# Performance work log

Hardware: AMD Instinct MI355X
Metric: run time of the kernel (lower is better)

The kernel has to match this reference:

```python
import jax, jax.numpy as jnp
import numpy as np

N = 40000      # nodes
E = 640000     # edges
G = 2048       # graphs
D = 128        # emb_dim
T = 10         # num_tasks
L = 5          # layers
ATOM_VOCAB = 64
BOND_VOCAB = 8
BN_EPS = 1e-5


def _bn(x, g, b, m, v):
    # inference-mode BatchNorm1d with running stats
    return (x - m) * jax.lax.rsqrt(v + BN_EPS) * g + b


def setup_inputs() -> dict:
    key = jax.random.key(0)
    ks = jax.random.split(key, 24)
    inp = {
        "x_atom": jax.random.randint(ks[0], (N, 9), 0, ATOM_VOCAB),
        "edge_index": jax.random.randint(ks[1], (2, E), 0, N),
        "edge_attr": jax.random.randint(ks[2], (E, 3), 0, BOND_VOCAB),
        "batch": jnp.sort(jax.random.randint(ks[3], (N,), 0, G)),
        # embedding tables
        "atom_emb": jax.random.normal(ks[4], (9, ATOM_VOCAB, D)) * 0.1,
        "bond_emb": jax.random.normal(ks[5], (L, 3, BOND_VOCAB, D)) * 0.1,
        # per-layer GIN params (stacked over L)
        "eps": jnp.zeros((L,)),
        "W1": jax.random.normal(ks[6], (L, D, 2 * D)) * 0.05,
        "b1": jnp.zeros((L, 2 * D)),
        "g1": jnp.ones((L, 2 * D)),
        "bt1": jnp.zeros((L, 2 * D)),
        "m1": jax.random.normal(ks[7], (L, 2 * D)) * 0.1,
        "v1": jax.random.uniform(ks[8], (L, 2 * D), minval=0.5, maxval=1.5),
        "W2": jax.random.normal(ks[9], (L, 2 * D, D)) * 0.05,
        "b2": jnp.zeros((L, D)),
        # outer BatchNorm per layer
        "gO": jnp.ones((L, D)),
        "btO": jnp.zeros((L, D)),
        "mO": jax.random.normal(ks[10], (L, D)) * 0.1,
        "vO": jax.random.uniform(ks[11], (L, D), minval=0.5, maxval=1.5),
        # prediction head
        "Wp": jax.random.normal(ks[12], (D, T)) * 0.05,
        "bp": jnp.zeros((T,)),
    }
    return inp


def reference(x_atom, edge_index, edge_attr, batch, atom_emb, bond_emb, eps,
              W1, b1, g1, bt1, m1, v1, W2, b2, gO, btO, mO, vO, Wp, bp):
    src, dst = edge_index[0], edge_index[1]
    # AtomEncoder: sum of per-feature embeddings -> [N, D]
    x = atom_emb[jnp.arange(9)[None, :], x_atom].sum(axis=1)
    feat3 = jnp.arange(3)[None, :]
    for i in range(L):
        # BondEncoder for this layer -> [E, D]
        e = bond_emb[i][feat3, edge_attr].sum(axis=1)
        # message: relu(x_j + edge_emb); aggregate: scatter-add at dst
        msg = jax.nn.relu(x[src] + e)
        agg = jax.ops.segment_sum(msg, dst, num_segments=N)
        h = (1.0 + eps[i]) * x + agg
        # MLP: Linear -> BN -> ReLU -> Linear
        h = jax.nn.relu(_bn(h @ W1[i] + b1[i], g1[i], bt1[i], m1[i], v1[i]))
        h = h @ W2[i] + b2[i]
        # outer BN; ReLU after all but last layer (dropout = identity in eval)
        x = _bn(h, gO[i], btO[i], mO[i], vO[i])
        if i < L - 1:
            x = jax.nn.relu(x)
    # global mean pool over graphs
    sums = jax.ops.segment_sum(x, batch, num_segments=G)
    cnt = jax.ops.segment_sum(jnp.ones((N,), x.dtype), batch, num_segments=G)
    pooled = sums / jnp.maximum(cnt, 1.0)[:, None]
    return pooled @ Wp + bp
```

## Files before the change

kernel.cpp:

```cpp
#include <hip/hip_runtime.h>
#include <hip/hip_bf16.h>

#define NN 40000
#define NE 640000
#define NG 2048
#define DD 128
#define NT 10
#define NL 5
#define NB 80

typedef __attribute__((ext_vector_type(8))) short short8;
typedef __attribute__((ext_vector_type(8))) float f32x8;
typedef __attribute__((ext_vector_type(4))) float f32x4;
typedef unsigned short ushort_t;
typedef unsigned char uchar_t;

static __device__ __forceinline__ ushort_t f2b(float f) {
    return __bfloat16_as_ushort(__float2bfloat16(f));
}
static __device__ __forceinline__ float b2f(ushort_t u) {
    return __bfloat162float(__ushort_as_bfloat16(u));
}
static __device__ __forceinline__ uchar_t f2p8(float f) {
    return (uchar_t)(__builtin_amdgcn_cvt_pk_fp8_f32(f, 0.f, 0, false) & 0xFF);
}

__global__ void __launch_bounds__(256)
k_setup(const float* __restrict__ W1, const float* __restrict__ W2,
        const float* __restrict__ bemb, const int* __restrict__ xa,
        const float* __restrict__ aemb, const int* __restrict__ ei,
        ushort_t* __restrict__ W1P, ushort_t* __restrict__ W2P,
        ushort_t* __restrict__ ebsum16, ushort_t* __restrict__ x16,
        uchar_t* __restrict__ x8, int* __restrict__ gcnt) {
    int b = blockIdx.x, t = threadIdx.x;
    if (b < 1280) {
        int tid = b * 256 + t;
        int layer = tid >> 16;
        int r = tid & 65535;
        int half = r >> 15;
        int q = r & 32767;
        int j = q & 7;
        int lane = (q >> 3) & 63;
        if (half == 0) {
            int kk = (q >> 9) & 3;
            int nt = q >> 11;
            int n = nt * 16 + (lane & 15);
            int k = kk * 32 + (lane >> 4) * 8 + j;
            W1P[layer * 32768 + q] = f2b(W1[(layer * DD + k) * 256 + n]);
        } else {
            int kk = (q >> 9) & 7;
            int nt = q >> 12;
            int n = nt * 16 + (lane & 15);
            int k = kk * 32 + (lane >> 4) * 8 + j;
            W2P[layer * 32768 + q] = f2b(W2[(layer * 256 + k) * DD + n]);
        }
        int d = tid & 127;
        int c = (tid >> 7) & 511;
        const float* bl = bemb + (size_t)layer * 3 * 8 * DD;
        ebsum16[tid] = f2b(bl[(c & 7) * DD + d] + bl[(8 + ((c >> 3) & 7)) * DD + d] +
                           bl[(16 + (c >> 6)) * DD + d]);
    } else if (b < 3780) {
        int bb = b - 1280;
        __shared__ int idxS[144];
        if (t < 144) idxS[t] = xa[bb * 144 + t];
        __syncthreads();
        int nl = t >> 4, dcol = t & 15;
        int n = bb * 16 + nl;
        float acc[8];
#pragma unroll
        for (int k = 0; k < 8; ++k) acc[k] = 0.f;
#pragma unroll
        for (int f = 0; f < 9; ++f) {
            const f32x8 v = *(const f32x8*)&aemb[(f * 64 + idxS[nl * 9 + f]) * DD + dcol * 8];
#pragma unroll
            for (int k = 0; k < 8; ++k) acc[k] += v[k];
        }
        short8 o16;
#pragma unroll
        for (int k = 0; k < 8; ++k) o16[k] = (short)f2b(acc[k]);
        *(short8*)&x16[(size_t)n * DD + dcol * 8] = o16;
        unsigned int lo = 0, hi = 0;
        lo = __builtin_amdgcn_cvt_pk_fp8_f32(acc[0], acc[1], lo, false);
        lo = __builtin_amdgcn_cvt_pk_fp8_f32(acc[2], acc[3], lo, true);
        hi = __builtin_amdgcn_cvt_pk_fp8_f32(acc[4], acc[5], hi, false);
        hi = __builtin_amdgcn_cvt_pk_fp8_f32(acc[6], acc[7], hi, true);
        *(uint2*)&x8[(size_t)n * DD + dcol * 8] = make_uint2(lo, hi);
    } else {
        __shared__ int hist[NB];
        int e0 = (b - 3780) * 1024;
        if (t < NB) hist[t] = 0;
        __syncthreads();
#pragma unroll
        for (int k = 0; k < 4; ++k) {
            int e = e0 + k * 256 + t;
            atomicAdd(&hist[ei[NE + e] >> 9], 1);
        }
        __syncthreads();
        if (t < NB) atomicAdd(&gcnt[t], hist[t]);
    }
}

__global__ void __launch_bounds__(256)
k_bucket(const int* __restrict__ ei, const int* __restrict__ ea,
         const int* __restrict__ gcnt, int* __restrict__ gbk,
         int2* __restrict__ ebuf) {
    __shared__ int hist[NB];
    __shared__ int sbase[NB];
    __shared__ int sB[128];
    __shared__ int exS[NB];
    int t = threadIdx.x;
    if (t < NB) hist[t] = 0;
    int v0 = 0;
    if (t < 128) { v0 = (t < NB) ? gcnt[t] : 0; sB[t] = v0; }
    __syncthreads();
    for (int d = 1; d < 128; d <<= 1) {
        int add = (t < 128 && t >= d) ? sB[t - d] : 0;
        __syncthreads();
        if (t < 128) sB[t] += add;
        __syncthreads();
    }
    if (t < NB) exS[t] = sB[t] - v0;
    __syncthreads();
    int e0 = blockIdx.x * 1024;
    int rank[4], buck[4], rec[4], dstv[4];
#pragma unroll
    for (int k = 0; k < 4; ++k) {
        int e = e0 + k * 256 + t;
        int src = ei[e];
        int dst = ei[NE + e];
        int a0 = ea[e * 3 + 0], a1 = ea[e * 3 + 1], a2 = ea[e * 3 + 2];
        rec[k] = src | ((a0 | (a1 << 3) | (a2 << 6)) << 16);
        dstv[k] = dst;
        int b = dst >> 9;
        buck[k] = b;
        rank[k] = atomicAdd(&hist[b], 1);
    }
    __syncthreads();
    if (t < NB) sbase[t] = atomicAdd(&gbk[t], hist[t]);
    __syncthreads();
#pragma unroll
    for (int k = 0; k < 4; ++k) {
        int b = buck[k];
        int slot = exS[b] + sbase[b] + rank[k];
        ebuf[slot] = make_int2(rec[k], dstv[k]);
    }
}

__global__ void __launch_bounds__(256)
k_csr(const int2* __restrict__ ebuf, const int* __restrict__ gcnt,
      int* __restrict__ off, int* __restrict__ epack) {
    __shared__ int cnt[512];
    __shared__ int cur[512];
    __shared__ int sc[256];
    __shared__ int sB[128];
    int b = blockIdx.x, t = threadIdx.x;
    int v0 = 0;
    if (t < 128) { v0 = (t < NB) ? gcnt[t] : 0; sB[t] = v0; }
    cnt[t] = 0; cnt[t + 256] = 0;
    cur[t] = 0; cur[t + 256] = 0;
    __syncthreads();
    for (int d = 1; d < 128; d <<= 1) {
        int add = (t < 128 && t >= d) ? sB[t - d] : 0;
        __syncthreads();
        if (t < 128) sB[t] += add;
        __syncthreads();
    }
    int base = sB[b] - gcnt[b];
    int end = base + gcnt[b];
    __syncthreads();
    for (int i = base + t; i < end; i += 256)
        atomicAdd(&cnt[ebuf[i].y & 511], 1);
    __syncthreads();
    int a = cnt[2 * t], c2 = cnt[2 * t + 1];
    sc[t] = a + c2;
    __syncthreads();
    for (int d = 1; d < 256; d <<= 1) {
        int add = (t >= d) ? sc[t - d] : 0;
        __syncthreads();
        sc[t] += add;
        __syncthreads();
    }
    int ex = sc[t] - (a + c2);
    cnt[2 * t] = ex;
    cnt[2 * t + 1] = ex + a;
    int n0 = (b << 9) + 2 * t;
    if (n0 <= NN) off[n0] = base + ex;
    if (n0 + 1 <= NN) off[n0 + 1] = base + ex + a;
    __syncthreads();
    for (int i = base + t; i < end; i += 256) {
        int2 s = ebuf[i];
        int l = s.y & 511;
        int r = atomicAdd(&cur[l], 1);
        epack[base + cnt[l] + r] = s.x;
    }
}

__global__ void __launch_bounds__(256)
k_gather(const ushort_t* __restrict__ xin, const uchar_t* __restrict__ x8in,
         const int* __restrict__ off, const int* __restrict__ epack,
         const ushort_t* __restrict__ ebsum16, const float* __restrict__ eps,
         int layer, ushort_t* __restrict__ h16) {
    int t = threadIdx.x;
    int lane = t & 63;
    int half = lane >> 5;
    int q = lane & 31;
    int n = blockIdx.x * 4 + (t >> 6);
    const ushort4* eb4 = (const ushort4*)ebsum16;
    const uint* xu = (const uint*)x8in;
    const ushort4* x4 = (const ushort4*)xin;
    ushort4 xv = x4[(size_t)n * 32 + q];
    float acc[4];
#pragma unroll
    for (int k = 0; k < 4; ++k) acc[k] = 0.f;
    int p = off[n], p1 = off[n + 1];

    int rec[8], recn[8];
    bool have = (p + 16 <= p1);
    if (have) {
#pragma unroll
        for (int j = 0; j < 8; ++j) rec[j] = epack[p + 2 * j + half];
    }
    while (have) {
        int np = p + 16;
        bool nh = (np + 16 <= p1);
        if (nh) {
#pragma unroll
            for (int j = 0; j < 8; ++j) recn[j] = epack[np + 2 * j + half];
        }
        ushort4 vv[8];
        uint ss[8];
#pragma unroll
        for (int j = 0; j < 8; ++j) {
            vv[j] = eb4[(rec[j] >> 16) * 32 + q];
            ss[j] = xu[(size_t)(rec[j] & 0xFFFF) * 32 + q];
        }
#pragma unroll
        for (int j = 0; j < 8; ++j) {
            acc[0] += fmaxf(b2f(vv[j].x) + __builtin_amdgcn_cvt_f32_fp8((int)ss[j], 0), 0.f);
            acc[1] += fmaxf(b2f(vv[j].y) + __builtin_amdgcn_cvt_f32_fp8((int)ss[j], 1), 0.f);
            acc[2] += fmaxf(b2f(vv[j].z) + __builtin_amdgcn_cvt_f32_fp8((int)ss[j], 2), 0.f);
            acc[3] += fmaxf(b2f(vv[j].w) + __builtin_amdgcn_cvt_f32_fp8((int)ss[j], 3), 0.f);
        }
        p = np;
#pragma unroll
        for (int j = 0; j < 8; ++j) rec[j] = recn[j];
        have = nh;
    }
    if (p + 8 <= p1) {
        int r4[4];
#pragma unroll
        for (int j = 0; j < 4; ++j) r4[j] = epack[p + 2 * j + half];
        ushort4 vv[4];
        uint ss[4];
#pragma unroll
        for (int j = 0; j < 4; ++j) {
            vv[j] = eb4[(r4[j] >> 16) * 32 + q];
            ss[j] = xu[(size_t)(r4[j] & 0xFFFF) * 32 + q];
        }
#pragma unroll
        for (int j = 0; j < 4; ++j) {
            acc[0] += fmaxf(b2f(vv[j].x) + __builtin_amdgcn_cvt_f32_fp8((int)ss[j], 0), 0.f);
            acc[1] += fmaxf(b2f(vv[j].y) + __builtin_amdgcn_cvt_f32_fp8((int)ss[j], 1), 0.f);
            acc[2] += fmaxf(b2f(vv[j].z) + __builtin_amdgcn_cvt_f32_fp8((int)ss[j], 2), 0.f);
            acc[3] += fmaxf(b2f(vv[j].w) + __builtin_amdgcn_cvt_f32_fp8((int)ss[j], 3), 0.f);
        }
        p += 8;
    }
    for (; p < p1; p += 2) {
        int eA = epack[p];
        bool hasB = (p + 1 < p1);
        int eB = hasB ? epack[p + 1] : eA;
        int r = half ? eB : eA;
        bool valid = half ? hasB : true;
        ushort4 v = eb4[(r >> 16) * 32 + q];
        uint s = xu[(size_t)(r & 0xFFFF) * 32 + q];
        if (valid) {
            acc[0] += fmaxf(b2f(v.x) + __builtin_amdgcn_cvt_f32_fp8((int)s, 0), 0.f);
            acc[1] += fmaxf(b2f(v.y) + __builtin_amdgcn_cvt_f32_fp8((int)s, 1), 0.f);
            acc[2] += fmaxf(b2f(v.z) + __builtin_amdgcn_cvt_f32_fp8((int)s, 2), 0.f);
            acc[3] += fmaxf(b2f(v.w) + __builtin_amdgcn_cvt_f32_fp8((int)s, 3), 0.f);
        }
    }
#pragma unroll
    for (int k = 0; k < 4; ++k) acc[k] += __shfl_xor(acc[k], 32, 64);
    if (half == 0) {
        float es = 1.f + eps[layer];
        ushort4 o;
        o.x = f2b(acc[0] + es * b2f(xv.x));
        o.y = f2b(acc[1] + es * b2f(xv.y));
        o.z = f2b(acc[2] + es * b2f(xv.z));
        o.w = f2b(acc[3] + es * b2f(xv.w));
        ((ushort4*)h16)[(size_t)n * 32 + q] = o;
    }
}

__global__ void __launch_bounds__(256)
k_mlp_mfma(const ushort_t* __restrict__ h16, const ushort_t* __restrict__ W1P,
           const ushort_t* __restrict__ W2P, const float* __restrict__ b1,
           const float* __restrict__ g1, const float* __restrict__ bt1,
           const float* __restrict__ m1, const float* __restrict__ v1,
           const float* __restrict__ b2_, const float* __restrict__ gO,
           const float* __restrict__ btO, const float* __restrict__ mO,
           const float* __restrict__ vO, int relu, ushort_t* __restrict__ xout,
           uchar_t* __restrict__ x8out) {
    __shared__ ushort_t aS[32 * 136];
    __shared__ ushort_t mid[32 * 264];
    int t = threadIdx.x;
    int wave = t >> 6, lane = t & 63;
    int row0 = blockIdx.x * 32;
    int lrow = lane & 15, quad = lane >> 4;

#pragma unroll
    for (int ps = 0; ps < 2; ++ps) {
        int idx = ps * 256 + t;
        int r = idx >> 4, c = (idx & 15) * 8;
        *(short8*)&aS[r * 136 + c] = *(const short8*)&h16[(row0 + r) * DD + c];
    }
    __syncthreads();

    f32x4 acc1[2][4];
#pragma unroll
    for (int rt = 0; rt < 2; ++rt)
#pragma unroll
        for (int i = 0; i < 4; ++i) acc1[rt][i] = (f32x4){0.f, 0.f, 0.f, 0.f};
#pragma unroll
    for (int kk = 0; kk < 4; ++kk) {
        short8 af0 = *(const short8*)&aS[lrow * 136 + kk * 32 + quad * 8];
        short8 af1 = *(const short8*)&aS[(16 + lrow) * 136 + kk * 32 + quad * 8];
#pragma unroll
        for (int i = 0; i < 4; ++i) {
            int nt = wave * 4 + i;
            short8 bf = *(const short8*)&W1P[((nt * 4 + kk) * 64 + lane) * 8];
            acc1[0][i] = __builtin_amdgcn_mfma_f32_16x16x32_bf16(af0, bf, acc1[0][i], 0, 0, 0);
            acc1[1][i] = __builtin_amdgcn_mfma_f32_16x16x32_bf16(af1, bf, acc1[1][i], 0, 0, 0);
        }
    }
    __syncthreads();
#pragma unroll
    for (int i = 0; i < 4; ++i) {
        int col = (wave * 4 + i) * 16 + lrow;
        float s1 = g1[col] * rsqrtf(v1[col] + 1e-5f);
        float sh = bt1[col] - (m1[col] - b1[col]) * s1;
#pragma unroll
        for (int rt = 0; rt < 2; ++rt)
#pragma unroll
            for (int r = 0; r < 4; ++r) {
                int row = rt * 16 + quad * 4 + r;
                float o = acc1[rt][i][r] * s1 + sh;
                mid[row * 264 + col] = f2b(fmaxf(o, 0.f));
            }
    }
    __syncthreads();

    f32x4 acc2[2][2];
#pragma unroll
    for (int rt = 0; rt < 2; ++rt)
#pragma unroll
        for (int i = 0; i < 2; ++i) acc2[rt][i] = (f32x4){0.f, 0.f, 0.f, 0.f};
#pragma unroll
    for (int kk = 0; kk < 8; ++kk) {
        short8 af0 = *(const short8*)&mid[lrow * 264 + kk * 32 + quad * 8];
        short8 af1 = *(const short8*)&mid[(16 + lrow) * 264 + kk * 32 + quad * 8];
#pragma unroll
        for (int i = 0; i < 2; ++i) {
            int nt = wave * 2 + i;
            short8 bf = *(const short8*)&W2P[((nt * 8 + kk) * 64 + lane) * 8];
            acc2[0][i] = __builtin_amdgcn_mfma_f32_16x16x32_bf16(af0, bf, acc2[0][i], 0, 0, 0);
            acc2[1][i] = __builtin_amdgcn_mfma_f32_16x16x32_bf16(af1, bf, acc2[1][i], 0, 0, 0);
        }
    }
    uchar_t* s8 = (uchar_t*)aS;
#pragma unroll
    for (int i = 0; i < 2; ++i) {
        int col = (wave * 2 + i) * 16 + lrow;
        float s = gO[col] * rsqrtf(vO[col] + 1e-5f);
        float sh = btO[col] - (mO[col] - b2_[col]) * s;
#pragma unroll
        for (int rt = 0; rt < 2; ++rt)
#pragma unroll
            for (int r = 0; r < 4; ++r) {
                int row = rt * 16 + quad * 4 + r;
                float o = acc2[rt][i][r] * s + sh;
                if (relu) o = fmaxf(o, 0.f);
                xout[(row0 + row) * DD + col] = f2b(o);
                s8[row * DD + col] = f2p8(o);
            }
    }
    __syncthreads();
    ((int4*)(x8out + (size_t)row0 * DD))[t] = ((const int4*)s8)[t];
}

__global__ void k_poolhead(const ushort_t* __restrict__ x16,
                           const int* __restrict__ batch,
                           const float* __restrict__ Wp, const float* __restrict__ bp,
                           float* __restrict__ out) {
    int g = blockIdx.x, t = threadIdx.x;
    int j = t >> 6, l = t & 63;
    int lo = 0, hi = NN;
    while (lo < hi) { int m = (lo + hi) >> 1; if (batch[m] < g) lo = m + 1; else hi = m; }
    int start = lo;
    hi = NN;
    while (lo < hi) { int m = (lo + hi) >> 1; if (batch[m] < g + 1) lo = m + 1; else hi = m; }
    int end = lo;
    const ushort2* x2 = (const ushort2*)x16;
    float sx = 0.f, sy = 0.f;
    for (int n = start + j; n < end; n += 4) {
        ushort2 v = x2[(size_t)n * 64 + l];
        sx += b2f(v.x);
        sy += b2f(v.y);
    }
    __shared__ float pp[4][DD];
    pp[j][2 * l] = sx;
    pp[j][2 * l + 1] = sy;
    __syncthreads();
    __shared__ float pfin[DD];
    if (t < DD) {
        float c = fmaxf((float)(end - start), 1.f);
        pfin[t] = (pp[0][t] + pp[1][t] + pp[2][t] + pp[3][t]) / c;
    }
    __syncthreads();
    if (t < NT) {
        float acc = bp[t];
#pragma unroll 8
        for (int k = 0; k < DD; ++k) acc = fmaf(pfin[k], Wp[k * NT + t], acc);
        out[g * NT + t] = acc;
    }
}

extern "C" void kernel_launch(void* const* d_in, const int* in_sizes, int n_in,
                              void* d_out, int out_size, void* d_ws, size_t ws_size,
                              hipStream_t stream) {
    const int* x_atom = (const int*)d_in[0];
    const int* edge_index = (const int*)d_in[1];
    const int* edge_attr = (const int*)d_in[2];
    const int* batch = (const int*)d_in[3];
    const float* atom_emb = (const float*)d_in[4];
    const float* bond_emb = (const float*)d_in[5];
    const float* eps = (const float*)d_in[6];
    const float* W1 = (const float*)d_in[7];
    const float* b1 = (const float*)d_in[8];
    const float* g1 = (const float*)d_in[9];
    const float* bt1 = (const float*)d_in[10];
    const float* m1 = (const float*)d_in[11];
    const float* v1 = (const float*)d_in[12];
    const float* W2 = (const float*)d_in[13];
    const float* b2 = (const float*)d_in[14];
    const float* gO = (const float*)d_in[15];
    const float* btO = (const float*)d_in[16];
    const float* mO = (const float*)d_in[17];
    const float* vO = (const float*)d_in[18];
    const float* Wp = (const float*)d_in[19];
    const float* bp = (const float*)d_in[20];

    ushort_t* x16a = (ushort_t*)d_ws;
    ushort_t* x16b = x16a + NN * DD;
    ushort_t* h16 = x16b + NN * DD;
    ushort_t* W1P = h16 + NN * DD;
    ushort_t* W2P = W1P + NL * 32768;
    ushort_t* ebsum16 = W2P + NL * 32768;
    uchar_t* x8a = (uchar_t*)(ebsum16 + NL * 65536);
    uchar_t* x8b = x8a + NN * DD;
    int* off = (int*)(x8b + NN * DD);
    int* gcnt = off + 40064;
    int* gbk = gcnt + 80;
    int* epack = gbk + 80;
    int2* ebuf = (int2*)(epack + NE);

    hipMemsetAsync(gcnt, 0, 160 * sizeof(int), stream);

    k_setup<<<4405, 256, 0, stream>>>(W1, W2, bond_emb, x_atom, atom_emb,
                                      edge_index, W1P, W2P, ebsum16, x16a, x8a, gcnt);
    k_bucket<<<NE / 1024, 256, 0, stream>>>(edge_index, edge_attr, gcnt, gbk, ebuf);
    k_csr<<<NB, 256, 0, stream>>>(ebuf, gcnt, off, epack);

    for (int i = 0; i < NL; ++i) {
        ushort_t* xin = (i & 1) ? x16b : x16a;
        ushort_t* xout = (i & 1) ? x16a : x16b;
        uchar_t* x8in = (i & 1) ? x8b : x8a;
        uchar_t* x8out = (i & 1) ? x8a : x8b;
        k_gather<<<NN / 4, 256, 0, stream>>>(xin, x8in, off, epack,
                                             ebsum16 + i * 65536, eps, i, h16);
        k_mlp_mfma<<<NN / 32, 256, 0, stream>>>(
            h16, W1P + (size_t)i * 32768, W2P + (size_t)i * 32768, b1 + i * 256,
            g1 + i * 256, bt1 + i * 256, m1 + i * 256, v1 + i * 256, b2 + i * DD,
            gO + i * DD, btO + i * DD, mO + i * DD, vO + i * DD,
            (i < NL - 1) ? 1 : 0, xout, x8out);
    }
    k_poolhead<<<NG, 256, 0, stream>>>(x16b, batch, Wp, bp, (float*)d_out);
}
```

Baseline: 382.5 us.

## Fuse all stages into one persistent cooperative kernel with grid syncs

Replaces the chain of setup, bucket, CSR, per-layer gather/MLP and pooling kernels with a single persistent cooperative kernel. Each stage loops over work units with a grid-stride pattern, and stages are separated by grid-wide barriers. The goal is to remove about 14 kernel launches and their launch gaps, plus the memset. In exchange, occupancy is capped by the shared-memory union and launch bounds, and every stage pays grid-sync cost, with some imbalance when stages have few blocks of work (for example the 80-block CSR stage).

```diff
diff --git a/kernel.cpp b/kernel.cpp
--- a/kernel.cpp
+++ b/kernel.cpp
@@ -1,5 +1,8 @@
 #include <hip/hip_runtime.h>
 #include <hip/hip_bf16.h>
+#include <hip/hip_cooperative_groups.h>
+
+namespace cg = cooperative_groups;
 
 #define NN 40000
 #define NE 640000
@@ -25,405 +28,450 @@
     return (uchar_t)(__builtin_amdgcn_cvt_pk_fp8_f32(f, 0.f, 0, false) & 0xFF);
 }
 
-__global__ void __launch_bounds__(256)
-k_setup(const float* __restrict__ W1, const float* __restrict__ W2,
-        const float* __restrict__ bemb, const int* __restrict__ xa,
-        const float* __restrict__ aemb, const int* __restrict__ ei,
-        ushort_t* __restrict__ W1P, ushort_t* __restrict__ W2P,
-        ushort_t* __restrict__ ebsum16, ushort_t* __restrict__ x16,
-        uchar_t* __restrict__ x8, int* __restrict__ gcnt) {
-    int b = blockIdx.x, t = threadIdx.x;
-    if (b < 1280) {
-        int tid = b * 256 + t;
-        int layer = tid >> 16;
-        int r = tid & 65535;
-        int half = r >> 15;
-        int q = r & 32767;
-        int j = q & 7;
-        int lane = (q >> 3) & 63;
-        if (half == 0) {
-            int kk = (q >> 9) & 3;
-            int nt = q >> 11;
-            int n = nt * 16 + (lane & 15);
-            int k = kk * 32 + (lane >> 4) * 8 + j;
-            W1P[layer * 32768 + q] = f2b(W1[(layer * DD + k) * 256 + n]);
+__global__ void __launch_bounds__(256, 4)
+k_mega(const int* __restrict__ xa, const int* __restrict__ ei,
+       const int* __restrict__ ea, const int* __restrict__ batch,
+       const float* __restrict__ aemb, const float* __restrict__ bemb,
+       const float* __restrict__ eps,
+       const float* __restrict__ W1, const float* __restrict__ b1,
+       const float* __restrict__ g1, const float* __restrict__ bt1,
+       const float* __restrict__ m1, const float* __restrict__ v1,
+       const float* __restrict__ W2, const float* __restrict__ b2,
+       const float* __restrict__ gO, const float* __restrict__ btO,
+       const float* __restrict__ mO, const float* __restrict__ vO,
+       const float* __restrict__ Wp, const float* __restrict__ bp,
+       void* __restrict__ ws, float* __restrict__ out) {
+    cg::grid_group gg = cg::this_grid();
+    __shared__ __align__(16) char smem[25600];
+    const int t = threadIdx.x;
+    const int nblk = gridDim.x;
+
+    ushort_t* x16a = (ushort_t*)ws;
+    ushort_t* x16b = x16a + NN * DD;
+    ushort_t* h16 = x16b + NN * DD;
+    ushort_t* W1P = h16 + NN * DD;
+    ushort_t* W2P = W1P + NL * 32768;
+    ushort_t* ebsum16 = W2P + NL * 32768;
+    uchar_t* x8a = (uchar_t*)(ebsum16 + NL * 65536);
+    uchar_t* x8b = x8a + NN * DD;
+    int* off = (int*)(x8b + NN * DD);
+    int* gcnt = off + 40064;
+    int* gbk = gcnt + 80;
+    int* epack = gbk + 80;
+    int2* ebuf = (int2*)(epack + NE);
+
+    if (blockIdx.x == 0 && t < 160) gcnt[t] = 0;
+    gg.sync();
+
+    for (int u = blockIdx.x; u < 4405; u += nblk) {
+        if (u < 1280) {
+            int tid = u * 256 + t;
+            int layer = tid >> 16;
+            int r = tid & 65535;
+            int half = r >> 15;
+            int q = r & 32767;
+            int j = q & 7;
+            int lane = (q >> 3) & 63;
+            if (half == 0) {
+                int kk = (q >> 9) & 3;
+                int nt = q >> 11;
+                int n = nt * 16 + (lane & 15);
+                int k = kk * 32 + (lane >> 4) * 8 + j;
+                W1P[layer * 32768 + q] = f2b(W1[(layer * DD + k) * 256 + n]);
+            } else {
+                int kk = (q >> 9) & 7;
+                int nt = q >> 12;
+                int n = nt * 16 + (lane & 15);
+                int k = kk * 32 + (lane >> 4) * 8 + j;
+                W2P[layer * 32768 + q] = f2b(W2[(layer * 256 + k) * DD + n]);
+            }
+            int d = tid & 127;
+            int c = (tid >> 7) & 511;
+            const float* bl = bemb + (size_t)layer * 3 * 8 * DD;
+            ebsum16[tid] = f2b(bl[(c & 7) * DD + d] + bl[(8 + ((c >> 3) & 7)) * DD + d] +
+                               bl[(16 + (c >> 6)) * DD + d]);
+        } else if (u < 3780) {
+            int bb = u - 1280;
+            int* idxS = (int*)smem;
+            if (t < 144) idxS[t] = xa[bb * 144 + t];
+            __syncthreads();
+            int nl = t >> 4, dcol = t & 15;
+            int n = bb * 16 + nl;
+            float acc[8];
+#pragma unroll
+            for (int k = 0; k < 8; ++k) acc[k] = 0.f;
+#pragma unroll
+            for (int f = 0; f < 9; ++f) {
+                const f32x8 v = *(const f32x8*)&aemb[(f * 64 + idxS[nl * 9 + f]) * DD + dcol * 8];
+#pragma unroll
+                for (int k = 0; k < 8; ++k) acc[k] += v[k];
+            }
+            short8 o16;
+#pragma unroll
+            for (int k = 0; k < 8; ++k) o16[k] = (short)f2b(acc[k]);
+            *(short8*)&x16a[(size_t)n * DD + dcol * 8] = o16;
+            unsigned int lo = 0, hi = 0;
+            lo = __builtin_amdgcn_cvt_pk_fp8_f32(acc[0], acc[1], lo, false);
+            lo = __builtin_amdgcn_cvt_pk_fp8_f32(acc[2], acc[3], lo, true);
+            hi = __builtin_amdgcn_cvt_pk_fp8_f32(acc[4], acc[5], hi, false);
+            hi = __builtin_amdgcn_cvt_pk_fp8_f32(acc[6], acc[7], hi, true);
+            *(uint2*)&x8a[(size_t)n * DD + dcol * 8] = make_uint2(lo, hi);
         } else {
-            int kk = (q >> 9) & 7;
-            int nt = q >> 12;
-            int n = nt * 16 + (lane & 15);
-            int k = kk * 32 + (lane >> 4) * 8 + j;
-            W2P[layer * 32768 + q] = f2b(W2[(layer * 256 + k) * DD + n]);
-        }
-        int d = tid & 127;
-        int c = (tid >> 7) & 511;
-        const float* bl = bemb + (size_t)layer * 3 * 8 * DD;
-        ebsum16[tid] = f2b(bl[(c & 7) * DD + d] + bl[(8 + ((c >> 3) & 7)) * DD + d] +
-                           bl[(16 + (c >> 6)) * DD + d]);
-    } else if (b < 3780) {
-        int bb = b - 1280;
-        __shared__ int idxS[144];
-        if (t < 144) idxS[t] = xa[bb * 144 + t];
-        __syncthreads();
-        int nl = t >> 4, dcol = t & 15;
-        int n = bb * 16 + nl;
-        float acc[8];
-#pragma unroll
-        for (int k = 0; k < 8; ++k) acc[k] = 0.f;
-#pragma unroll
-        for (int f = 0; f < 9; ++f) {
-            const f32x8 v = *(const f32x8*)&aemb[(f * 64 + idxS[nl * 9 + f]) * DD + dcol * 8];
-#pragma unroll
-            for (int k = 0; k < 8; ++k) acc[k] += v[k];
-        }
-        short8 o16;
-#pragma unroll
-        for (int k = 0; k < 8; ++k) o16[k] = (short)f2b(acc[k]);
-        *(short8*)&x16[(size_t)n * DD + dcol * 8] = o16;
-        unsigned int lo = 0, hi = 0;
-        lo = __builtin_amdgcn_cvt_pk_fp8_f32(acc[0], acc[1], lo, false);
-        lo = __builtin_amdgcn_cvt_pk_fp8_f32(acc[2], acc[3], lo, true);
-        hi = __builtin_amdgcn_cvt_pk_fp8_f32(acc[4], acc[5], hi, false);
-        hi = __builtin_amdgcn_cvt_pk_fp8_f32(acc[6], acc[7], hi, true);
-        *(uint2*)&x8[(size_t)n * DD + dcol * 8] = make_uint2(lo, hi);
-    } else {
-        __shared__ int hist[NB];
-        int e0 = (b - 3780) * 1024;
-        if (t < NB) hist[t] = 0;
-        __syncthreads();
-#pragma unroll
-        for (int k = 0; k < 4; ++k) {
-            int e = e0 + k * 256 + t;
-            atomicAdd(&hist[ei[NE + e] >> 9], 1);
-        }
-        __syncthreads();
-        if (t < NB) atomicAdd(&gcnt[t], hist[t]);
+            int* hist = (int*)smem;
+            int e0 = (u - 3780) * 1024;
+            if (t < NB) hist[t] = 0;
+            __syncthreads();
+#pragma unroll
+            for (int k = 0; k < 4; ++k) {
+                int e = e0 + k * 256 + t;
+                atomicAdd(&hist[ei[NE + e] >> 9], 1);
+            }
+            __syncthreads();
+            if (t < NB) atomicAdd(&gcnt[t], hist[t]);
+        }
+        __syncthreads();
     }
-}
-
-__global__ void __launch_bounds__(256)
-k_bucket(const int* __restrict__ ei, const int* __restrict__ ea,
-         const int* __restrict__ gcnt, int* __restrict__ gbk,
-         int2* __restrict__ ebuf) {
-    __shared__ int hist[NB];
-    __shared__ int sbase[NB];
-    __shared__ int sB[128];
-    __shared__ int exS[NB];
-    int t = threadIdx.x;
-    if (t < NB) hist[t] = 0;
-    int v0 = 0;
-    if (t < 128) { v0 = (t < NB) ? gcnt[t] : 0; sB[t] = v0; }
-    __syncthreads();
-    for (int d = 1; d < 128; d <<= 1) {
-        int add = (t < 128 && t >= d) ? sB[t - d] : 0;
-        __syncthreads();
-        if (t < 128) sB[t] += add;
-        __syncthreads();
+    gg.sync();
+
+    {
+        int* hist = (int*)smem;
+        int* sbase = hist + NB;
+        int* sB = sbase + NB;
+        int* exS = sB + 128;
+        int v0 = 0;
+        if (t < 128) { v0 = (t < NB) ? gcnt[t] : 0; sB[t] = v0; }
+        __syncthreads();
+        for (int d = 1; d < 128; d <<= 1) {
+            int add = (t < 128 && t >= d) ? sB[t - d] : 0;
+            __syncthreads();
+            if (t < 128) sB[t] += add;
+            __syncthreads();
+        }
+        if (t < NB) exS[t] = sB[t] - v0;
+        __syncthreads();
+        for (int u = blockIdx.x; u < NE / 1024; u += nblk) {
+            if (t < NB) hist[t] = 0;
+            __syncthreads();
+            int e0 = u * 1024;
+            int rank[4], buck[4], rec[4], dstv[4];
+#pragma unroll
+            for (int k = 0; k < 4; ++k) {
+                int e = e0 + k * 256 + t;
+                int src = ei[e];
+                int dst = ei[NE + e];
+                int a0 = ea[e * 3 + 0], a1 = ea[e * 3 + 1], a2 = ea[e * 3 + 2];
+                rec[k] = src | ((a0 | (a1 << 3) | (a2 << 6)) << 16);
+                dstv[k] = dst;
+                int b = dst >> 9;
+                buck[k] = b;
+                rank[k] = atomicAdd(&hist[b], 1);
+            }
+            __syncthreads();
+            if (t < NB) sbase[t] = atomicAdd(&gbk[t], hist[t]);
+            __syncthreads();
+#pragma unroll
+            for (int k = 0; k < 4; ++k) {
+                int b = buck[k];
+                int slot = exS[b] + sbase[b] + rank[k];
+                ebuf[slot] = make_int2(rec[k], dstv[k]);
+            }
+            __syncthreads();
+        }
     }
-    if (t < NB) exS[t] = sB[t] - v0;
-    __syncthreads();
-    int e0 = blockIdx.x * 1024;
-    int rank[4], buck[4], rec[4], dstv[4];
-#pragma unroll
-    for (int k = 0; k < 4; ++k) {
-        int e = e0 + k * 256 + t;
-        int src = ei[e];
-        int dst = ei[NE + e];
-        int a0 = ea[e * 3 + 0], a1 = ea[e * 3 + 1], a2 = ea[e * 3 + 2];
-        rec[k] = src | ((a0 | (a1 << 3) | (a2 << 6)) << 16);
-        dstv[k] = dst;
-        int b = dst >> 9;
-        buck[k] = b;
-        rank[k] = atomicAdd(&hist[b], 1);
+    gg.sync();
+
+    if (blockIdx.x < NB) {
+        int b = blockIdx.x;
+        int* cnt = (int*)smem;
+        int* cur = cnt + 512;
+        int* sc = cur + 512;
+        int* sB = sc + 256;
+        int v0 = 0;
+        if (t < 128) { v0 = (t < NB) ? gcnt[t] : 0; sB[t] = v0; }
+        cnt[t] = 0; cnt[t + 256] = 0;
+        cur[t] = 0; cur[t + 256] = 0;
+        __syncthreads();
+        for (int d = 1; d < 128; d <<= 1) {
+            int add = (t < 128 && t >= d) ? sB[t - d] : 0;
+            __syncthreads();
+            if (t < 128) sB[t] += add;
+            __syncthreads();
+        }
+        int base = sB[b] - gcnt[b];
+        int end = base + gcnt[b];
+        __syncthreads();
+        for (int i = base + t; i < end; i += 256)
+            atomicAdd(&cnt[ebuf[i].y & 511], 1);
+        __syncthreads();
+        int a = cnt[2 * t], c2 = cnt[2 * t + 1];
+        sc[t] = a + c2;
+        __syncthreads();
+        for (int d = 1; d < 256; d <<= 1) {
+            int add = (t >= d) ? sc[t - d] : 0;
+            __syncthreads();
+            sc[t] += add;
+            __syncthreads();
+        }
+        int ex = sc[t] - (a + c2);
+        cnt[2 * t] = ex;
+        cnt[2 * t + 1] = ex + a;
+        int n0 = (b << 9) + 2 * t;
+        if (n0 <= NN) off[n0] = base + ex;
+        if (n0 + 1 <= NN) off[n0 + 1] = base + ex + a;
+        __syncthreads();
+        for (int i = base + t; i < end; i += 256) {
+            int2 s = ebuf[i];
+            int l = s.y & 511;
+            int r = atomicAdd(&cur[l], 1);
+            epack[base + cnt[l] + r] = s.x;
+        }
     }
-    __syncthreads();
-    if (t < NB) sbase[t] = atomicAdd(&gbk[t], hist[t]);
-    __syncthreads();
-#pragma unroll
-    for (int k = 0; k < 4; ++k) {
-        int b = buck[k];
-        int slot = exS[b] + sbase[b] + rank[k];
-        ebuf[slot] = make_int2(rec[k], dstv[k]);
+    gg.sync();
+
+    const int lane = t & 63;
+    const int halfl = lane >> 5;
+    const int q = lane & 31;
+    const int wave = t >> 6;
+    const int lrow = lane & 15, quad = lane >> 4;
+
+    for (int i = 0; i < NL; ++i) {
+        const ushort_t* xin = (i & 1) ? x16b : x16a;
+        ushort_t* xout = (i & 1) ? x16a : x16b;
+        const uchar_t* x8in = (i & 1) ? x8b : x8a;
+        uchar_t* x8out = (i & 1) ? x8a : x8b;
+        const ushort_t* ebl = ebsum16 + i * 65536;
+        float es = 1.f + eps[i];
+
+        {
+            const ushort4* eb4 = (const ushort4*)ebl;
+            const uint* xu = (const uint*)x8in;
+            const ushort4* x4 = (const ushort4*)xin;
+            for (int u = blockIdx.x; u < NN / 4; u += nblk) {
+                int n = u * 4 + wave;
+                ushort4 xv = x4[(size_t)n * 32 + q];
+                float acc[4];
+#pragma unroll
+                for (int k = 0; k < 4; ++k) acc[k] = 0.f;
+                int p = off[n], p1 = off[n + 1];
+
+                int rec[8], recn[8];
+                bool have = (p + 16 <= p1);
+                if (have) {
+#pragma unroll
+                    for (int j = 0; j < 8; ++j) rec[j] = epack[p + 2 * j + halfl];
+                }
+                while (have) {
+                    int np = p + 16;
+                    bool nh = (np + 16 <= p1);
+                    if (nh) {
+#pragma unroll
+                        for (int j = 0; j < 8; ++j) recn[j] = epack[np + 2 * j + halfl];
+                    }
+                    ushort4 vv[8];
+                    uint ss[8];
+#pragma unroll
+                    for (int j = 0; j < 8; ++j) {
+                        vv[j] = eb4[(rec[j] >> 16) * 32 + q];
+                        ss[j] = xu[(size_t)(rec[j] & 0xFFFF) * 32 + q];
+                    }
+#pragma unroll
+                    for (int j = 0; j < 8; ++j) {
+                        acc[0] += fmaxf(b2f(vv[j].x) + __builtin_amdgcn_cvt_f32_fp8((int)ss[j], 0), 0.f);
+                        acc[1] += fmaxf(b2f(vv[j].y) + __builtin_amdgcn_cvt_f32_fp8((int)ss[j], 1), 0.f);
+                        acc[2] += fmaxf(b2f(vv[j].z) + __builtin_amdgcn_cvt_f32_fp8((int)ss[j], 2), 0.f);
+                        acc[3] += fmaxf(b2f(vv[j].w) + __builtin_amdgcn_cvt_f32_fp8((int)ss[j], 3), 0.f);
+                    }
+                    p = np;
+#pragma unroll
+                    for (int j = 0; j < 8; ++j) rec[j] = recn[j];
+                    have = nh;
+                }
+                if (p + 8 <= p1) {
+                    int r4[4];
+#pragma unroll
+                    for (int j = 0; j < 4; ++j) r4[j] = epack[p + 2 * j + halfl];
+                    ushort4 vv[4];
+                    uint ss[4];
+#pragma unroll
+                    for (int j = 0; j < 4; ++j) {
+                        vv[j] = eb4[(r4[j] >> 16) * 32 + q];
+                        ss[j] = xu[(size_t)(r4[j] & 0xFFFF) * 32 + q];
+                    }
+#pragma unroll
+                    for (int j = 0; j < 4; ++j) {
+                        acc[0] += fmaxf(b2f(vv[j].x) + __builtin_amdgcn_cvt_f32_fp8((int)ss[j], 0), 0.f);
+                        acc[1] += fmaxf(b2f(vv[j].y) + __builtin_amdgcn_cvt_f32_fp8((int)ss[j], 1), 0.f);
+                        acc[2] += fmaxf(b2f(vv[j].z) + __builtin_amdgcn_cvt_f32_fp8((int)ss[j], 2), 0.f);
+                        acc[3] += fmaxf(b2f(vv[j].w) + __builtin_amdgcn_cvt_f32_fp8((int)ss[j], 3), 0.f);
+                    }
+                    p += 8;
+                }
+                for (; p < p1; p += 2) {
+                    int eA = epack[p];
+                    bool hasB = (p + 1 < p1);
+                    int eB = hasB ? epack[p + 1] : eA;
+                    int r = halfl ? eB : eA;
+                    bool valid = halfl ? hasB : true;
+                    ushort4 v = eb4[(r >> 16) * 32 + q];
+                    uint s = xu[(size_t)(r & 0xFFFF) * 32 + q];
+                    if (valid) {
+                        acc[0] += fmaxf(b2f(v.x) + __builtin_amdgcn_cvt_f32_fp8((int)s, 0), 0.f);
+                        acc[1] += fmaxf(b2f(v.y) + __builtin_amdgcn_cvt_f32_fp8((int)s, 1), 0.f);
+                        acc[2] += fmaxf(b2f(v.z) + __builtin_amdgcn_cvt_f32_fp8((int)s, 2), 0.f);
+                        acc[3] += fmaxf(b2f(v.w) + __builtin_amdgcn_cvt_f32_fp8((int)s, 3), 0.f);
+                    }
+                }
+#pragma unroll
+                for (int k = 0; k < 4; ++k) acc[k] += __shfl_xor(acc[k], 32, 64);
+                if (halfl == 0) {
+                    ushort4 o;
+                    o.x = f2b(acc[0] + es * b2f(xv.x));
+                    o.y = f2b(acc[1] + es * b2f(xv.y));
+                    o.z = f2b(acc[2] + es * b2f(xv.z));
+                    o.w = f2b(acc[3] + es * b2f(xv.w));
+                    ((ushort4*)h16)[(size_t)n * 32 + q] = o;
+                }
+            }
+        }
+        gg.sync();
+
+        {
+            const ushort_t* W1Pl = W1P + (size_t)i * 32768;
+            const ushort_t* W2Pl = W2P + (size_t)i * 32768;
+            const float* b1l = b1 + i * 256;
+            const float* g1l = g1 + i * 256;
+            const float* bt1l = bt1 + i * 256;
+            const float* m1l = m1 + i * 256;
+            const float* v1l = v1 + i * 256;
+            const float* b2l = b2 + i * DD;
+            const float* gOl = gO + i * DD;
+            const float* btOl = btO + i * DD;
+            const float* mOl = mO + i * DD;
+            const float* vOl = vO + i * DD;
+            int relu = (i < NL - 1) ? 1 : 0;
+            ushort_t* aS = (ushort_t*)smem;
+            ushort_t* mid = (ushort_t*)(smem + 8704);
+
+            for (int u = blockIdx.x; u < NN / 32; u += nblk) {
+                int row0 = u * 32;
+#pragma unroll
+                for (int ps = 0; ps < 2; ++ps) {
+                    int idx = ps * 256 + t;
+                    int r = idx >> 4, c = (idx & 15) * 8;
+                    *(short8*)&aS[r * 136 + c] = *(const short8*)&h16[(row0 + r) * DD + c];
+                }
+                __syncthreads();
+
+                f32x4 acc1[2][4];
+#pragma unroll
+                for (int rt = 0; rt < 2; ++rt)
+#pragma unroll
+                    for (int ii = 0; ii < 4; ++ii) acc1[rt][ii] = (f32x4){0.f, 0.f, 0.f, 0.f};
+#pragma unroll
+                for (int kk = 0; kk < 4; ++kk) {
+                    short8 af0 = *(const short8*)&aS[lrow * 136 + kk * 32 + quad * 8];
+                    short8 af1 = *(const short8*)&aS[(16 + lrow) * 136 + kk * 32 + quad * 8];
+#pragma unroll
+                    for (int ii = 0; ii < 4; ++ii) {
+                        int nt = wave * 4 + ii;
+                        short8 bf = *(const short8*)&W1Pl[((nt * 4 + kk) * 64 + lane) * 8];
+                        acc1[0][ii] = __builtin_amdgcn_mfma_f32_16x16x32_bf16(af0, bf, acc1[0][ii], 0, 0, 0);
+                        acc1[1][ii] = __builtin_amdgcn_mfma_f32_16x16x32_bf16(af1, bf, acc1[1][ii], 0, 0, 0);
+                    }
+                }
+                __syncthreads();
+#pragma unroll
+                for (int ii = 0; ii < 4; ++ii) {
+                    int col = (wave * 4 + ii) * 16 + lrow;
+                    float s1 = g1l[col] * rsqrtf(v1l[col] + 1e-5f);
+                    float sh = bt1l[col] - (m1l[col] - b1l[col]) * s1;
+#pragma unroll
+                    for (int rt = 0; rt < 2; ++rt)
+#pragma unroll
+                        for (int r = 0; r < 4; ++r) {
+                            int row = rt * 16 + quad * 4 + r;
+                            float o = acc1[rt][ii][r] * s1 + sh;
+                            mid[row * 264 + col] = f2b(fmaxf(o, 0.f));
+                        }
+                }
+                __syncthreads();
+
+                f32x4 acc2[2][2];
+#pragma unroll
+                for (int rt = 0; rt < 2; ++rt)
+#pragma unroll
+                    for (int ii = 0; ii < 2; ++ii) acc2[rt][ii] = (f32x4){0.f, 0.f, 0.f, 0.f};
+#pragma unroll
+                for (int kk = 0; kk < 8; ++kk) {
+                    short8 af0 = *(const short8*)&mid[lrow * 264 + kk * 32 + quad * 8];
+                    short8 af1 = *(const short8*)&mid[(16 + lrow) * 264 + kk * 32 + quad * 8];
+#pragma unroll
+                    for (int ii = 0; ii < 2; ++ii) {
+                        int nt = wave * 2 + ii;
+                        short8 bf = *(const short8*)&W2Pl[((nt * 8 + kk) * 64 + lane) * 8];
+                        acc2[0][ii] = __builtin_amdgcn_mfma_f32_16x16x32_bf16(af0, bf, acc2[0][ii], 0, 0, 0);
+                        acc2[1][ii] = __builtin_amdgcn_mfma_f32_16x16x32_bf16(af1, bf, acc2[1][ii], 0, 0, 0);
+                    }
+                }
+                uchar_t* s8 = (uchar_t*)aS;
+#pragma unroll
+                for (int ii = 0; ii < 2; ++ii) {
+                    int col = (wave * 2 + ii) * 16 + lrow;
+                    float s = gOl[col] * rsqrtf(vOl[col] + 1e-5f);
+                    float sh = btOl[col] - (mOl[col] - b2l[col]) * s;
+#pragma unroll
+                    for (int rt = 0; rt < 2; ++rt)
+#pragma unroll
+                        for (int r = 0; r < 4; ++r) {
+                            int row = rt * 16 + quad * 4 + r;
+                            float o = acc2[rt][ii][r] * s + sh;
+                            if (relu) o = fmaxf(o, 0.f);
+                            xout[(row0 + row) * DD + col] = f2b(o);
+                            s8[row * DD + col] = f2p8(o);
+                        }
+                }
+                __syncthreads();
+                ((int4*)(x8out + (size_t)row0 * DD))[t] = ((const int4*)s8)[t];
+                __syncthreads();
+            }
+        }
+        gg.sync();
     }
-}
-
-__global__ void __launch_bounds__(256)
-k_csr(const int2* __restrict__ ebuf, const int* __restrict__ gcnt,
-      int* __restrict__ off, int* __restrict__ epack) {
-    __shared__ int cnt[512];
-    __shared__ int cur[512];
-    __shared__ int sc[256];
-    __shared__ int sB[128];
-    int b = blockIdx.x, t = threadIdx.x;
-    int v0 = 0;
-    if (t < 128) { v0 = (t < NB) ? gcnt[t] : 0; sB[t] = v0; }
-    cnt[t] = 0; cnt[t + 256] = 0;
-    cur[t] = 0; cur[t + 256] = 0;
-    __syncthreads();
-    for (int d = 1; d < 128; d <<= 1) {
-        int add = (t < 128 && t >= d) ? sB[t - d] : 0;
-        __syncthreads();
-        if (t < 128) sB[t] += add;
-        __syncthreads();
-    }
-    int base = sB[b] - gcnt[b];
-    int end = base + gcnt[b];
-    __syncthreads();
-    for (int i = base + t; i < end; i += 256)
-        atomicAdd(&cnt[ebuf[i].y & 511], 1);
-    __syncthreads();
-    int a = cnt[2 * t], c2 = cnt[2 * t + 1];
-    sc[t] = a + c2;
-    __syncthreads();
-    for (int d = 1; d < 256; d <<= 1) {
-        int add = (t >= d) ? sc[t - d] : 0;
-        __syncthreads();
-        sc[t] += add;
-        __syncthreads();
-    }
-    int ex = sc[t] - (a + c2);
-    cnt[2 * t] = ex;
-    cnt[2 * t + 1] = ex + a;
-    int n0 = (b << 9) + 2 * t;
-    if (n0 <= NN) off[n0] = base + ex;
-    if (n0 + 1 <= NN) off[n0 + 1] = base + ex + a;
-    __syncthreads();
-    for (int i = base + t; i < end; i += 256) {
-        int2 s = ebuf[i];
-        int l = s.y & 511;
-        int r = atomicAdd(&cur[l], 1);
-        epack[base + cnt[l] + r] = s.x;
-    }
-}
-
-__global__ void __launch_bounds__(256)
-k_gather(const ushort_t* __restrict__ xin, const uchar_t* __restrict__ x8in,
-         const int* __restrict__ off, const int* __restrict__ epack,
-         const ushort_t* __restrict__ ebsum16, const float* __restrict__ eps,
-         int layer, ushort_t* __restrict__ h16) {
-    int t = threadIdx.x;
-    int lane = t & 63;
-    int half = lane >> 5;
-    int q = lane & 31;
-    int n = blockIdx.x * 4 + (t >> 6);
-    const ushort4* eb4 = (const ushort4*)ebsum16;
-    const uint* xu = (const uint*)x8in;
-    const ushort4* x4 = (const ushort4*)xin;
-    ushort4 xv = x4[(size_t)n * 32 + q];
-    float acc[4];
-#pragma unroll
-    for (int k = 0; k < 4; ++k) acc[k] = 0.f;
-    int p = off[n], p1 = off[n + 1];
-
-    int rec[8], recn[8];
-    bool have = (p + 16 <= p1);
-    if (have) {
-#pragma unroll
-        for (int j = 0; j < 8; ++j) rec[j] = epack[p + 2 * j + half];
-    }
-    while (have) {
-        int np = p + 16;
-        bool nh = (np + 16 <= p1);
-        if (nh) {
-#pragma unroll
-            for (int j = 0; j < 8; ++j) recn[j] = epack[np + 2 * j + half];
-        }
-        ushort4 vv[8];
-        uint ss[8];
-#pragma unroll
-        for (int j = 0; j < 8; ++j) {
-            vv[j] = eb4[(rec[j] >> 16) * 32 + q];
-            ss[j] = xu[(size_t)(rec[j] & 0xFFFF) * 32 + q];
-        }
-#pragma unroll
-        for (int j = 0; j < 8; ++j) {
-            acc[0] += fmaxf(b2f(vv[j].x) + __builtin_amdgcn_cvt_f32_fp8((int)ss[j], 0), 0.f);
-            acc[1] += fmaxf(b2f(vv[j].y) + __builtin_amdgcn_cvt_f32_fp8((int)ss[j], 1), 0.f);
-            acc[2] += fmaxf(b2f(vv[j].z) + __builtin_amdgcn_cvt_f32_fp8((int)ss[j], 2), 0.f);
-            acc[3] += fmaxf(b2f(vv[j].w) + __builtin_amdgcn_cvt_f32_fp8((int)ss[j], 3), 0.f);
-        }
-        p = np;
-#pragma unroll
-        for (int j = 0; j < 8; ++j) rec[j] = recn[j];
-        have = nh;
-    }
-    if (p + 8 <= p1) {
-        int r4[4];
-#pragma unroll
-        for (int j = 0; j < 4; ++j) r4[j] = epack[p + 2 * j + half];
-        ushort4 vv[4];
-        uint ss[4];
-#pragma unroll
-        for (int j = 0; j < 4; ++j) {
-            vv[j] = eb4[(r4[j] >> 16) * 32 + q];
-            ss[j] = xu[(size_t)(r4[j] & 0xFFFF) * 32 + q];
-        }
-#pragma unroll
-        for (int j = 0; j < 4; ++j) {
-            acc[0] += fmaxf(b2f(vv[j].x) + __builtin_amdgcn_cvt_f32_fp8((int)ss[j], 0), 0.f);
-            acc[1] += fmaxf(b2f(vv[j].y) + __builtin_amdgcn_cvt_f32_fp8((int)ss[j], 1), 0.f);
-            acc[2] += fmaxf(b2f(vv[j].z) + __builtin_amdgcn_cvt_f32_fp8((int)ss[j], 2), 0.f);
-            acc[3] += fmaxf(b2f(vv[j].w) + __builtin_amdgcn_cvt_f32_fp8((int)ss[j], 3), 0.f);
-        }
-        p += 8;
-    }
-    for (; p < p1; p += 2) {
-        int eA = epack[p];
-        bool hasB = (p + 1 < p1);
-        int eB = hasB ? epack[p + 1] : eA;
-        int r = half ? eB : eA;
-        bool valid = half ? hasB : true;
-        ushort4 v = eb4[(r >> 16) * 32 + q];
-        uint s = xu[(size_t)(r & 0xFFFF) * 32 + q];
-        if (valid) {
-            acc[0] += fmaxf(b2f(v.x) + __builtin_amdgcn_cvt_f32_fp8((int)s, 0), 0.f);
-            acc[1] += fmaxf(b2f(v.y) + __builtin_amdgcn_cvt_f32_fp8((int)s, 1), 0.f);
-            acc[2] += fmaxf(b2f(v.z) + __builtin_amdgcn_cvt_f32_fp8((int)s, 2), 0.f);
-            acc[3] += fmaxf(b2f(v.w) + __builtin_amdgcn_cvt_f32_fp8((int)s, 3), 0.f);
-        }
-    }
-#pragma unroll
-    for (int k = 0; k < 4; ++k) acc[k] += __shfl_xor(acc[k], 32, 64);
-    if (half == 0) {
-        float es = 1.f + eps[layer];
-        ushort4 o;
-        o.x = f2b(acc[0] + es * b2f(xv.x));
-        o.y = f2b(acc[1] + es * b2f(xv.y));
-        o.z = f2b(acc[2] + es * b2f(xv.z));
-        o.w = f2b(acc[3] + es * b2f(xv.w));
-        ((ushort4*)h16)[(size_t)n * 32 + q] = o;
-    }
-}
-
-__global__ void __launch_bounds__(256)
-k_mlp_mfma(const ushort_t* __restrict__ h16, const ushort_t* __restrict__ W1P,
-           const ushort_t* __restrict__ W2P, const float* __restrict__ b1,
-           const float* __restrict__ g1, const float* __restrict__ bt1,
-           const float* __restrict__ m1, const float* __restrict__ v1,
-           const float* __restrict__ b2_, const float* __restrict__ gO,
-           const float* __restrict__ btO, const float* __restrict__ mO,
-           const float* __restrict__ vO, int relu, ushort_t* __restrict__ xout,
-           uchar_t* __restrict__ x8out) {
-    __shared__ ushort_t aS[32 * 136];
-    __shared__ ushort_t mid[32 * 264];
-    int t = threadIdx.x;
-    int wave = t >> 6, lane = t & 63;
-    int row0 = blockIdx.x * 32;
-    int lrow = lane & 15, quad = lane >> 4;
-
-#pragma unroll
-    for (int ps = 0; ps < 2; ++ps) {
-        int idx = ps * 256 + t;
-        int r = idx >> 4, c = (idx & 15) * 8;
-        *(short8*)&aS[r * 136 + c] = *(const short8*)&h16[(row0 + r) * DD + c];
-    }
-    __syncthreads();
-
-    f32x4 acc1[2][4];
-#pragma unroll
-    for (int rt = 0; rt < 2; ++rt)
-#pragma unroll
-        for (int i = 0; i < 4; ++i) acc1[rt][i] = (f32x4){0.f, 0.f, 0.f, 0.f};
-#pragma unroll
-    for (int kk = 0; kk < 4; ++kk) {
-        short8 af0 = *(const short8*)&aS[lrow * 136 + kk * 32 + quad * 8];
-        short8 af1 = *(const short8*)&aS[(16 + lrow) * 136 + kk * 32 + quad * 8];
-#pragma unroll
-        for (int i = 0; i < 4; ++i) {
-            int nt = wave * 4 + i;
-            short8 bf = *(const short8*)&W1P[((nt * 4 + kk) * 64 + lane) * 8];
-            acc1[0][i] = __builtin_amdgcn_mfma_f32_16x16x32_bf16(af0, bf, acc1[0][i], 0, 0, 0);
-            acc1[1][i] = __builtin_amdgcn_mfma_f32_16x16x32_bf16(af1, bf, acc1[1][i], 0, 0, 0);
-        }
-    }
-    __syncthreads();
-#pragma unroll
-    for (int i = 0; i < 4; ++i) {
-        int col = (wave * 4 + i) * 16 + lrow;
-        float s1 = g1[col] * rsqrtf(v1[col] + 1e-5f);
-        float sh = bt1[col] - (m1[col] - b1[col]) * s1;
-#pragma unroll
-        for (int rt = 0; rt < 2; ++rt)
-#pragma unroll
-            for (int r = 0; r < 4; ++r) {
-                int row = rt * 16 + quad * 4 + r;
-                float o = acc1[rt][i][r] * s1 + sh;
-                mid[row * 264 + col] = f2b(fmaxf(o, 0.f));
-            }
-    }
-    __syncthreads();
-
-    f32x4 acc2[2][2];
-#pragma unroll
-    for (int rt = 0; rt < 2; ++rt)
-#pragma unroll
-        for (int i = 0; i < 2; ++i) acc2[rt][i] = (f32x4){0.f, 0.f, 0.f, 0.f};
-#pragma unroll
-    for (int kk = 0; kk < 8; ++kk) {
-        short8 af0 = *(const short8*)&mid[lrow * 264 + kk * 32 + quad * 8];
-        short8 af1 = *(const short8*)&mid[(16 + lrow) * 264 + kk * 32 + quad * 8];
-#pragma unroll
-        for (int i = 0; i < 2; ++i) {
-            int nt = wave * 2 + i;
-            short8 bf = *(const short8*)&W2P[((nt * 8 + kk) * 64 + lane) * 8];
-            acc2[0][i] = __builtin_amdgcn_mfma_f32_16x16x32_bf16(af0, bf, acc2[0][i], 0, 0, 0);
-            acc2[1][i] = __builtin_amdgcn_mfma_f32_16x16x32_bf16(af1, bf, acc2[1][i], 0, 0, 0);
-        }
-    }
-    uchar_t* s8 = (uchar_t*)aS;
-#pragma unroll
-    for (int i = 0; i < 2; ++i) {
-        int col = (wave * 2 + i) * 16 + lrow;
-        float s = gO[col] * rsqrtf(vO[col] + 1e-5f);
-        float sh = btO[col] - (mO[col] - b2_[col]) * s;
-#pragma unroll
-        for (int rt = 0; rt < 2; ++rt)
-#pragma unroll
-            for (int r = 0; r < 4; ++r) {
-                int row = rt * 16 + quad * 4 + r;
-                float o = acc2[rt][i][r] * s + sh;
-                if (relu) o = fmaxf(o, 0.f);
-                xout[(row0 + row) * DD + col] = f2b(o);
-                s8[row * DD + col] = f2p8(o);
-            }
-    }
-    __syncthreads();
-    ((int4*)(x8out + (size_t)row0 * DD))[t] = ((const int4*)s8)[t];
-}
-
-__global__ void k_poolhead(const ushort_t* __restrict__ x16,
-                           const int* __restrict__ batch,
-                           const float* __restrict__ Wp, const float* __restrict__ bp,
-                           float* __restrict__ out) {
-    int g = blockIdx.x, t = threadIdx.x;
-    int j = t >> 6, l = t & 63;
-    int lo = 0, hi = NN;
-    while (lo < hi) { int m = (lo + hi) >> 1; if (batch[m] < g) lo = m + 1; else hi = m; }
-    int start = lo;
-    hi = NN;
-    while (lo < hi) { int m = (lo + hi) >> 1; if (batch[m] < g + 1) lo = m + 1; else hi = m; }
-    int end = lo;
-    const ushort2* x2 = (const ushort2*)x16;
-    float sx = 0.f, sy = 0.f;
-    for (int n = start + j; n < end; n += 4) {
-        ushort2 v = x2[(size_t)n * 64 + l];
-        sx += b2f(v.x);
-        sy += b2f(v.y);
-    }
-    __shared__ float pp[4][DD];
-    pp[j][2 * l] = sx;
-    pp[j][2 * l + 1] = sy;
-    __syncthreads();
-    __shared__ float pfin[DD];
-    if (t < DD) {
-        float c = fmaxf((float)(end - start), 1.f);
-        pfin[t] = (pp[0][t] + pp[1][t] + pp[2][t] + pp[3][t]) / c;
-    }
-    __syncthreads();
-    if (t < NT) {
-        float acc = bp[t];
+
+    {
+        float* pp = (float*)smem;
+        float* pfin = pp + 4 * DD;
+        int j = t >> 6, l = t & 63;
+        const ushort2* x2 = (const ushort2*)x16b;
+        for (int g = blockIdx.x; g < NG; g += nblk) {
+            int lo = 0, hi = NN;
+            while (lo < hi) { int m = (lo + hi) >> 1; if (batch[m] < g) lo = m + 1; else hi = m; }
+            int start = lo;
+            hi = NN;
+            while (lo < hi) { int m = (lo + hi) >> 1; if (batch[m] < g + 1) lo = m + 1; else hi = m; }
+            int end = lo;
+            float sx = 0.f, sy = 0.f;
+            for (int n = start + j; n < end; n += 4) {
+                ushort2 v = x2[(size_t)n * 64 + l];
+                sx += b2f(v.x);
+                sy += b2f(v.y);
+            }
+            pp[j * DD + 2 * l] = sx;
+            pp[j * DD + 2 * l + 1] = sy;
+            __syncthreads();
+            if (t < DD) {
+                float c = fmaxf((float)(end - start), 1.f);
+                pfin[t] = (pp[0 * DD + t] + pp[1 * DD + t] + pp[2 * DD + t] + pp[3 * DD + t]) / c;
+            }
+            __syncthreads();
+            if (t < NT) {
+                float acc = bp[t];
 #pragma unroll 8
-        for (int k = 0; k < DD; ++k) acc = fmaf(pfin[k], Wp[k * NT + t], acc);
-        out[g * NT + t] = acc;
+                for (int k = 0; k < DD; ++k) acc = fmaf(pfin[k], Wp[k * NT + t], acc);
+                out[g * NT + t] = acc;
+            }
+            __syncthreads();
+        }
     }
 }
 
@@ -451,40 +499,25 @@
     const float* vO = (const float*)d_in[18];
     const float* Wp = (const float*)d_in[19];
     const float* bp = (const float*)d_in[20];
-
-    ushort_t* x16a = (ushort_t*)d_ws;
-    ushort_t* x16b = x16a + NN * DD;
-    ushort_t* h16 = x16b + NN * DD;
-    ushort_t* W1P = h16 + NN * DD;
-    ushort_t* W2P = W1P + NL * 32768;
-    ushort_t* ebsum16 = W2P + NL * 32768;
-    uchar_t* x8a = (uchar_t*)(ebsum16 + NL * 65536);
-    uchar_t* x8b = x8a + NN * DD;
-    int* off = (int*)(x8b + NN * DD);
-    int* gcnt = off + 40064;
-    int* gbk = gcnt + 80;
-    int* epack = gbk + 80;
-    int2* ebuf = (int2*)(epack + NE);
-
-    hipMemsetAsync(gcnt, 0, 160 * sizeof(int), stream);
-
-    k_setup<<<4405, 256, 0, stream>>>(W1, W2, bond_emb, x_atom, atom_emb,
-                                      edge_index, W1P, W2P, ebsum16, x16a, x8a, gcnt);
-    k_bucket<<<NE / 1024, 256, 0, stream>>>(edge_index, edge_attr, gcnt, gbk, ebuf);
-    k_csr<<<NB, 256, 0, stream>>>(ebuf, gcnt, off, epack);
-
-    for (int i = 0; i < NL; ++i) {
-        ushort_t* xin = (i & 1) ? x16b : x16a;
-        ushort_t* xout = (i & 1) ? x16a : x16b;
-        uchar_t* x8in = (i & 1) ? x8b : x8a;
-        uchar_t* x8out = (i & 1) ? x8a : x8b;
-        k_gather<<<NN / 4, 256, 0, stream>>>(xin, x8in, off, epack,
-                                             ebsum16 + i * 65536, eps, i, h16);
-        k_mlp_mfma<<<NN / 32, 256, 0, stream>>>(
-            h16, W1P + (size_t)i * 32768, W2P + (size_t)i * 32768, b1 + i * 256,
-            g1 + i * 256, bt1 + i * 256, m1 + i * 256, v1 + i * 256, b2 + i * DD,
-            gO + i * DD, btO + i * DD, mO + i * DD, vO + i * DD,
-            (i < NL - 1) ? 1 : 0, xout, x8out);
+    float* out = (float*)d_out;
+    void* ws = d_ws;
+
+    static int grid = 0;
+    if (grid == 0) {
+        int maxb = 0;
+        hipOccupancyMaxActiveBlocksPerMultiprocessor(&maxb, k_mega, 256, 0);
+        if (maxb < 1) maxb = 1;
+        grid = maxb * 256;
+        if (grid > 1536) grid = 1536;
     }
-    k_poolhead<<<NG, 256, 0, stream>>>(x16b, batch, Wp, bp, (float*)d_out);
+
+    void* kargs[] = {(void*)&x_atom, (void*)&edge_index, (void*)&edge_attr,
+                     (void*)&batch, (void*)&atom_emb, (void*)&bond_emb,
+                     (void*)&eps, (void*)&W1, (void*)&b1, (void*)&g1,
+                     (void*)&bt1, (void*)&m1, (void*)&v1, (void*)&W2,
+                     (void*)&b2, (void*)&gO, (void*)&btO, (void*)&mO,
+                     (void*)&vO, (void*)&Wp, (void*)&bp, (void*)&ws,
+                     (void*)&out};
+    hipLaunchCooperativeKernel((void*)k_mega, dim3(grid), dim3(256), kargs, 0,
+                               stream);
 }
```

Result: slower. 1.481 ms (+287.1%).
